# Kernel tuning notes

Hardware: AMD Instinct MI355X
Metric: run time of the kernel (lower is better)

Reference implementation:

```python
import jax, jax.numpy as jnp
import numpy as np

EPS = float(np.finfo(np.float32).eps)


def _m_step(padded, shifted, gp, B, K, C):
    # padded: [u, b=C+1, i, j]; shifted: [u, s, a=C, i, j]; gp: [u, k, i, j]
    ops_first = jnp.einsum('usaij,ukij,ubij->uskab', shifted, gp, padded)
    ops_second = jnp.einsum('uaij,ukij,ubij->ukab', padded, gp, padded)
    norm = 1.0 / jnp.einsum('ukaa->uk', ops_second)  # reciprocal of trace
    ops_first_n = ops_first * norm[:, None, :, None, None]
    eye_b = jnp.eye(C + 1, dtype=padded.dtype)
    ops_second_n = ops_second * norm[:, :, None, None] + EPS * eye_b
    ops = jnp.einsum('uskab,ukbc->uskac', ops_first_n, jnp.linalg.inv(ops_second_n))
    probs_norm = 1.0 / gp.sum(axis=(2, 3))
    pp = gp * probs_norm[:, :, None, None]
    # difference: [u, s, k, a, i, j]
    diff = shifted[:, :, None] - jnp.einsum('uskab,ubij->uskaij', ops, padded)
    eye_a = jnp.eye(C, dtype=padded.dtype)
    sigmas = jnp.einsum('uskaij,ukij,uskbij->uskab', diff, pp, diff) + EPS * eye_a
    return ops, sigmas


def _e_step(padded, shifted, ops, sigmas, B, K):
    diff = shifted[:, :, None] - jnp.einsum('uskab,ubij->uskaij', ops, padded)
    quad = jnp.einsum('uskaij,uskab,uskbij->ukij', diff, jnp.linalg.inv(sigmas), diff)
    _, logdet = jnp.linalg.slogdet(sigmas)  # sigmas is PD -> sign=+1
    return -0.5 * quad - 0.5 * logdet.sum(axis=1).reshape(B, K, 1, 1)


def em_forward(images, shifted_images, predicted_masks, em_steps):
    B, S, C, H, W = shifted_images.shape
    K = predicted_masks.shape[1]
    ones = jnp.ones((B, 1, H, W), dtype=images.dtype)
    padded = jnp.concatenate((images, ones), axis=1)  # [u, C+1, i, j]
    generated_masks = jnp.zeros_like(predicted_masks)
    for _ in range(em_steps):
        logits = jax.lax.stop_gradient(predicted_masks + generated_masks)
        gp = jax.nn.softmax(logits, axis=1) + EPS
        ops, sigmas = _m_step(jax.lax.stop_gradient(padded),
                              jax.lax.stop_gradient(shifted_images), gp, B, K, C)
        ops = jax.lax.stop_gradient(ops)
        sigmas = jax.lax.stop_gradient(sigmas)
        generated_masks = _e_step(padded, shifted_images, ops, sigmas, B, K)
    return generated_masks


def setup_inputs() -> dict:
    key = jax.random.key(0)
    k1, k2, k3 = jax.random.split(key, 3)
    B, S, C, H, W, K = 16, 8, 3, 128, 128, 6
    images = jax.random.uniform(k1, (B, C, H, W), dtype=jnp.float32)
    shifted_images = jax.random.uniform(k2, (B, S, C, H, W), dtype=jnp.float32)
    predicted_masks = jax.random.normal(k3, (B, K, H, W), dtype=jnp.float32)
    return {"images": images, "shifted_images": shifted_images,
            "predicted_masks": predicted_masks}


def reference(images, shifted_images, predicted_masks):
    return em_forward(images, shifted_images, predicted_masks, em_steps=3)
```

## Files before the change

kernel.cpp:

```cpp
#include <hip/hip_runtime.h>
#include <math.h>

#define EPSF 1.1920928955078125e-07f

constexpr int B_ = 16, S_ = 8, CH = 3, K_ = 6;
constexpr int P_ = 128 * 128;
constexpr int NCR = 4;
constexpr int NCE = 32;
constexpr int NF = 160;
constexpr int PW = 168;

__device__ __forceinline__ int swz8(int bid, int nwg) {
  return (bid & 7) * (nwg >> 3) + (bid >> 3);
}
__device__ __forceinline__ float4 ld4(const float* p) { return *(const float4*)p; }
__device__ __forceinline__ void st4(float* p, float4 v) { *(float4*)p = v; }
__device__ __forceinline__ float dot4(float4 a, float4 b) {
  return a.x * b.x + a.y * b.y + a.z * b.z + a.w * b.w;
}
__device__ __forceinline__ float sum4(float4 a) { return a.x + a.y + a.z + a.w; }
__device__ __forceinline__ float4 mul4(float4 a, float4 b) {
  return make_float4(a.x * b.x, a.y * b.y, a.z * b.z, a.w * b.w);
}
__device__ __forceinline__ float4 dcompv(float4 s, float4 i0, float4 i1, float4 i2,
                                         float4 o) {
  float4 r;
  r.x = s.x - (o.x * i0.x + o.y * i1.x + o.z * i2.x + o.w);
  r.y = s.y - (o.x * i0.y + o.y * i1.y + o.z * i2.y + o.w);
  r.z = s.z - (o.x * i0.z + o.y * i1.z + o.z * i2.z + o.w);
  r.w = s.w - (o.x * i0.w + o.y * i1.w + o.z * i2.w + o.w);
  return r;
}
__device__ __forceinline__ float quadv(float d0, float d1, float d2, float4 sA,
                                       float2 sB) {
  return sA.x * d0 * d0 + sA.y * d0 * d1 + sA.z * d0 * d2 + sA.w * d1 * d1 +
         sB.x * d1 * d2 + sB.y * d2 * d2;
}

__device__ __forceinline__ void inv4(const float* Ain, float* out) {
  float a[4][8];
#pragma unroll
  for (int i = 0; i < 4; i++) {
#pragma unroll
    for (int j = 0; j < 4; j++) { a[i][j] = Ain[i * 4 + j]; a[i][4 + j] = (i == j) ? 1.f : 0.f; }
  }
#pragma unroll
  for (int c = 0; c < 4; c++) {
    float piv = 1.f / a[c][c];
#pragma unroll
    for (int j = 0; j < 8; j++) a[c][j] *= piv;
#pragma unroll
    for (int r = 0; r < 4; r++) {
      if (r != c) {
        float f = a[r][c];
#pragma unroll
        for (int j = 0; j < 8; j++) a[r][j] -= f * a[c][j];
      }
    }
  }
#pragma unroll
  for (int i = 0; i < 4; i++)
#pragma unroll
    for (int j = 0; j < 4; j++) out[i * 4 + j] = a[i][4 + j];
}

__global__ __launch_bounds__(256) void k_softmax0(const float* __restrict__ pred,
                                                  float* __restrict__ gp) {
  int g = blockIdx.x * 256 + threadIdx.x;
  int u = g >> 14, p = g & (P_ - 1);
  const float* pr = pred + ((size_t)u * K_) * P_ + p;
  float l[K_];
  float mx = -1e30f;
#pragma unroll
  for (int k = 0; k < K_; k++) { l[k] = pr[(size_t)k * P_]; mx = fmaxf(mx, l[k]); }
  float s = 0.f;
#pragma unroll
  for (int k = 0; k < K_; k++) { l[k] = expf(l[k] - mx); s += l[k]; }
  float inv = 1.f / s;
  float* gw = gp + ((size_t)u * K_) * P_ + p;
#pragma unroll
  for (int k = 0; k < K_; k++) gw[(size_t)k * P_] = l[k] * inv + EPSF;
}

__global__ __launch_bounds__(256, 1) void k_moments(const float* __restrict__ img,
                                                    const float* __restrict__ shf,
                                                    const float* __restrict__ gp,
                                                    float* __restrict__ p1) {
  __shared__ float red[46][33];
  int wg = swz8(blockIdx.x, B_ * K_ * 4 * NCR);
  int u = wg / 96;
  int r = wg % 96;
  int k = r >> 4, sq = (r >> 2) & 3, ch = r & 3;
  int tid = threadIdx.x, lane = tid & 63, w = tid >> 6;

  const float* imgu = img + (size_t)u * CH * P_;
  const float* shfu = shf + ((size_t)u * S_ + sq * 2) * CH * P_;
  const float* gpu = gp + (size_t)(u * K_ + k) * P_;

  float acc[46];
#pragma unroll
  for (int i = 0; i < 46; i++) acc[i] = 0.f;

#pragma unroll
  for (int it = 0; it < 4; it++) {
    int p = ch * 4096 + it * 1024 + tid * 4;
    float4 i0 = ld4(imgu + p);
    float4 i1 = ld4(imgu + P_ + p);
    float4 i2 = ld4(imgu + 2 * P_ + p);
    float4 g = ld4(gpu + p);
    float4 t0 = mul4(g, i0), t1 = mul4(g, i1), t2 = mul4(g, i2);
#pragma unroll
    for (int ls = 0; ls < 2; ls++) {
      float4 s0 = ld4(shfu + (ls * 3 + 0) * P_ + p);
      float4 s1 = ld4(shfu + (ls * 3 + 1) * P_ + p);
      float4 s2 = ld4(shfu + (ls * 3 + 2) * P_ + p);
      int fb = ls * 12;
      acc[fb + 0] += dot4(s0, t0); acc[fb + 1] += dot4(s0, t1);
      acc[fb + 2] += dot4(s0, t2); acc[fb + 3] += dot4(s0, g);
      acc[fb + 4] += dot4(s1, t0); acc[fb + 5] += dot4(s1, t1);
      acc[fb + 6] += dot4(s1, t2); acc[fb + 7] += dot4(s1, g);
      acc[fb + 8] += dot4(s2, t0); acc[fb + 9] += dot4(s2, t1);
      acc[fb + 10] += dot4(s2, t2); acc[fb + 11] += dot4(s2, g);
      float4 gs0 = mul4(g, s0), gs1 = mul4(g, s1), gs2 = mul4(g, s2);
      int mb = 24 + ls * 6;
      acc[mb + 0] += dot4(gs0, s0); acc[mb + 1] += dot4(gs0, s1);
      acc[mb + 2] += dot4(gs0, s2); acc[mb + 3] += dot4(gs1, s1);
      acc[mb + 4] += dot4(gs1, s2); acc[mb + 5] += dot4(gs2, s2);
    }
    if (sq == 0) {
      acc[36] += dot4(i0, t0); acc[37] += dot4(i1, t0); acc[38] += dot4(i2, t0);
      acc[39] += sum4(t0);
      acc[40] += dot4(i1, t1); acc[41] += dot4(i2, t1); acc[42] += sum4(t1);
      acc[43] += dot4(i2, t2); acc[44] += sum4(t2);
      acc[45] += sum4(g);
    }
  }
#pragma unroll
  for (int j = 0; j < 46; j++) {
    float v = acc[j];
    v += __shfl_xor(v, 1, 64);
    v += __shfl_xor(v, 2, 64);
    v += __shfl_xor(v, 4, 64);
    acc[j] = v;
  }
  if ((lane & 7) == 0) {
    int col = w * 8 + (lane >> 3);
#pragma unroll
    for (int j = 0; j < 46; j++) red[j][col] = acc[j];
  }
  __syncthreads();
  if (tid < 46 && (tid < 36 || sq == 0)) {
    float s = 0.f;
#pragma unroll
    for (int c = 0; c < 32; c++) s += red[tid][c];
    int off = (tid < 24) ? (sq * 24 + tid)
                         : (tid < 36 ? (106 + sq * 12 + tid - 24) : (96 + tid - 36));
    p1[((size_t)(u * K_ + k) * NCR + ch) * NF + off] = s;
  }
}

__global__ __launch_bounds__(256) void k_solve(const float* __restrict__ p1,
                                               float* __restrict__ params) {
  __shared__ float sumL[K_][154];
  __shared__ float invAL[K_][16];
  __shared__ float OL[K_][96];
  __shared__ float normL[K_], pnL[K_];
  __shared__ float ldetL[K_ * S_];
  int u = blockIdx.x;
  int tid = threadIdx.x;

  for (int e = tid; e < K_ * 154; e += 256) {
    int k = e / 154, i = e % 154;
    const float* src = p1 + (size_t)(u * K_ + k) * NCR * NF + i;
    float s = 0.f;
#pragma unroll
    for (int c = 0; c < NCR; c++) s += src[c * NF];
    sumL[k][i] = s;
  }
  __syncthreads();
  if (tid < K_) {
    const float* m = &sumL[tid][96];
    float tr = m[0] + m[4] + m[7] + m[9];
    float nrm = 1.f / tr;
    normL[tid] = nrm;
    pnL[tid] = 1.f / m[9];
    const int sym[4][4] = {{0, 1, 2, 3}, {1, 4, 5, 6}, {2, 5, 7, 8}, {3, 6, 8, 9}};
    float A[16];
#pragma unroll
    for (int i = 0; i < 4; i++)
#pragma unroll
      for (int j = 0; j < 4; j++)
        A[i * 4 + j] = m[sym[i][j]] * nrm + ((i == j) ? EPSF : 0.f);
    inv4(A, invAL[tid]);
  }
  __syncthreads();
  for (int e = tid; e < K_ * 96; e += 256) {
    int k = e / 96, r = e % 96, sa = r >> 2, bc = r & 3;
    float v = 0.f;
#pragma unroll
    for (int c = 0; c < 4; c++) v += sumL[k][sa * 4 + c] * invAL[k][c * 4 + bc];
    v *= normL[k];
    OL[k][r] = v;
    params[(size_t)(u * K_ + k) * PW + r] = v;
  }
  __syncthreads();
  if (tid < K_ * S_) {
    int k = tid >> 3, s = tid & 7;
    const float* F = &sumL[k][s * 12];
    const float* O = &OL[k][s * 12];
    const float* M2 = &sumL[k][96];
    const float* Ms = &sumL[k][106 + s * 6];
    float pn = pnL[k];
    const int sym[4][4] = {{0, 1, 2, 3}, {1, 4, 5, 6}, {2, 5, 7, 8}, {3, 6, 8, 9}};
    float FO[9];
#pragma unroll
    for (int a = 0; a < 3; a++)
#pragma unroll
      for (int b = 0; b < 3; b++) {
        float v = 0.f;
#pragma unroll
        for (int c = 0; c < 4; c++) v += F[a * 4 + c] * O[b * 4 + c];
        FO[a * 3 + b] = v;
      }
    float W[12];
#pragma unroll
    for (int a = 0; a < 3; a++)
#pragma unroll
      for (int c = 0; c < 4; c++) {
        float v = 0.f;
#pragma unroll
        for (int d = 0; d < 4; d++) v += O[a * 4 + d] * M2[sym[d][c]];
        W[a * 4 + c] = v;
      }
    float OMO[6];
    {
      const int pa[6] = {0, 0, 0, 1, 1, 2}, pb[6] = {0, 1, 2, 1, 2, 2};
#pragma unroll
      for (int t = 0; t < 6; t++) {
        float v = 0.f;
#pragma unroll
        for (int c = 0; c < 4; c++) v += W[pa[t] * 4 + c] * O[pb[t] * 4 + c];
        OMO[t] = v;
      }
    }
    float a = pn * (Ms[0] - 2.f * FO[0] + OMO[0]) + EPSF;
    float b = pn * (Ms[1] - FO[1] - FO[3] + OMO[1]);
    float c = pn * (Ms[2] - FO[2] - FO[6] + OMO[2]);
    float d = pn * (Ms[3] - 2.f * FO[4] + OMO[3]) + EPSF;
    float e = pn * (Ms[4] - FO[5] - FO[7] + OMO[4]);
    float f = pn * (Ms[5] - 2.f * FO[8] + OMO[5]) + EPSF;
    float c00 = d * f - e * e, c01 = c * e - b * f, c02 = b * e - c * d;
    float det = a * c00 + b * c01 + c * c02;
    float id = 1.f / det;
    float* ps = params + (size_t)(u * K_ + k) * PW + 96 + s * 8;
    ps[0] = 0.5f * c00 * id;
    ps[1] = c01 * id;
    ps[2] = c02 * id;
    ps[3] = 0.5f * (a * f - c * c) * id;
    ps[4] = (c * b - a * e) * id;
    ps[5] = 0.5f * (a * d - b * b) * id;
    ldetL[tid] = logf(det);
  }
  __syncthreads();
  if (tid < K_) {
    float s = 0.f;
#pragma unroll
    for (int si = 0; si < S_; si++) s += ldetL[tid * S_ + si];
    params[(size_t)(u * K_ + tid) * PW + 160] = 0.5f * s;
  }
}

template <int LAST>
__global__ __launch_bounds__(768, 3) void k_estep(const float* __restrict__ img,
                                                  const float* __restrict__ shf,
                                                  const float* __restrict__ pred,
                                                  const float* __restrict__ params,
                                                  float* __restrict__ out,
                                                  float* __restrict__ gp) {
  __shared__ __align__(16) float pL[K_][PW];
  __shared__ __align__(16) float qL[K_][512];
  __shared__ __align__(16) float gmL[K_][512];

  int wg = swz8(blockIdx.x, B_ * NCE);
  int u = wg >> 5, ch = wg & 31;
  int tid = threadIdx.x, lane = tid & 63, w = tid >> 6;
  int k = w >> 1, shalf = w & 1;

  for (int e = tid; e < K_ * PW; e += 768)
    pL[e / PW][e % PW] = params[(size_t)u * K_ * PW + e];
  __syncthreads();

  const float* ob = &pL[k][shalf * 48];
  const float* sb = &pL[k][96 + shalf * 32];
  float ldh = pL[k][160];

  const float* imgu = img + (size_t)u * CH * P_;
  const float* shfu = shf + ((size_t)u * S_ + shalf * 4) * CH * P_;

  int p0 = ch * 512 + lane * 4;
  float4 i0a = ld4(imgu + p0),          i0b = ld4(imgu + p0 + 256);
  float4 i1a = ld4(imgu + P_ + p0),     i1b = ld4(imgu + P_ + p0 + 256);
  float4 i2a = ld4(imgu + 2 * P_ + p0), i2b = ld4(imgu + 2 * P_ + p0 + 256);
  float4 qa = make_float4(0.f, 0.f, 0.f, 0.f);
  float4 qb = make_float4(0.f, 0.f, 0.f, 0.f);
#pragma unroll
  for (int sl = 0; sl < 4; sl++) {
    float4 oA = ld4(ob + sl * 12 + 0);
    float4 oB = ld4(ob + sl * 12 + 4);
    float4 oC = ld4(ob + sl * 12 + 8);
    float4 sA = ld4(sb + sl * 8);
    float2 sB = *(const float2*)(sb + sl * 8 + 4);
    const float* s0 = shfu + (sl * 3 + 0) * P_;
    const float* s1 = shfu + (sl * 3 + 1) * P_;
    const float* s2 = shfu + (sl * 3 + 2) * P_;
    {
      float4 d0 = dcompv(ld4(s0 + p0), i0a, i1a, i2a, oA);
      float4 d1 = dcompv(ld4(s1 + p0), i0a, i1a, i2a, oB);
      float4 d2 = dcompv(ld4(s2 + p0), i0a, i1a, i2a, oC);
      qa.x += quadv(d0.x, d1.x, d2.x, sA, sB);
      qa.y += quadv(d0.y, d1.y, d2.y, sA, sB);
      qa.z += quadv(d0.z, d1.z, d2.z, sA, sB);
      qa.w += quadv(d0.w, d1.w, d2.w, sA, sB);
    }
    {
      float4 d0 = dcompv(ld4(s0 + p0 + 256), i0b, i1b, i2b, oA);
      float4 d1 = dcompv(ld4(s1 + p0 + 256), i0b, i1b, i2b, oB);
      float4 d2 = dcompv(ld4(s2 + p0 + 256), i0b, i1b, i2b, oC);
      qb.x += quadv(d0.x, d1.x, d2.x, sA, sB);
      qb.y += quadv(d0.y, d1.y, d2.y, sA, sB);
      qb.z += quadv(d0.z, d1.z, d2.z, sA, sB);
      qb.w += quadv(d0.w, d1.w, d2.w, sA, sB);
    }
  }
  int pxa = lane * 4, pxb = lane * 4 + 256;
  if (shalf == 1) {
    st4(&qL[k][pxa], qa);
    st4(&qL[k][pxb], qb);
  }
  __syncthreads();
  if (shalf == 0) {
    float* outu = out + (size_t)(u * K_ + k) * P_;
    float4 qha = ld4(&qL[k][pxa]);
    float4 qhb = ld4(&qL[k][pxb]);
    float4 g4a, g4b;
    g4a.x = -(qa.x + qha.x + ldh); g4a.y = -(qa.y + qha.y + ldh);
    g4a.z = -(qa.z + qha.z + ldh); g4a.w = -(qa.w + qha.w + ldh);
    g4b.x = -(qb.x + qhb.x + ldh); g4b.y = -(qb.y + qhb.y + ldh);
    g4b.z = -(qb.z + qhb.z + ldh); g4b.w = -(qb.w + qhb.w + ldh);
    st4(outu + ch * 512 + pxa, g4a);
    st4(outu + ch * 512 + pxb, g4b);
    if constexpr (!LAST) {
      st4(&gmL[k][pxa], g4a);
      st4(&gmL[k][pxb], g4b);
    }
  }
  if constexpr (!LAST) {
    __syncthreads();
    if (tid < 512) {
      int p = ch * 512 + tid;
      const float* predu = pred + (size_t)u * K_ * P_;
      float* gpu = gp + (size_t)u * K_ * P_;
      float l[K_];
      float mx = -1e30f;
#pragma unroll
      for (int k2 = 0; k2 < K_; k2++) {
        l[k2] = predu[(size_t)k2 * P_ + p] + gmL[k2][tid];
        mx = fmaxf(mx, l[k2]);
      }
      float ss = 0.f;
#pragma unroll
      for (int k2 = 0; k2 < K_; k2++) { l[k2] = expf(l[k2] - mx); ss += l[k2]; }
      float inv = 1.f / ss;
#pragma unroll
      for (int k2 = 0; k2 < K_; k2++) gpu[(size_t)k2 * P_ + p] = l[k2] * inv + EPSF;
    }
  }
}

extern "C" void kernel_launch(void* const* d_in, const int* in_sizes, int n_in,
                              void* d_out, int out_size, void* d_ws, size_t ws_size,
                              hipStream_t stream) {
  const float* img = (const float*)d_in[0];
  const float* shf = (const float*)d_in[1];
  const float* pred = (const float*)d_in[2];
  float* out = (float*)d_out;
  float* wsf = (float*)d_ws;
  float* gp = wsf;
  float* p1 = gp + (size_t)B_ * K_ * P_;
  float* params = p1 + (size_t)B_ * K_ * NCR * NF;

  k_softmax0<<<(B_ * P_) / 256, 256, 0, stream>>>(pred, gp);
  for (int step = 0; step < 3; step++) {
    k_moments<<<B_ * K_ * 4 * NCR, 256, 0, stream>>>(img, shf, gp, p1);
    k_solve<<<B_, 256, 0, stream>>>(p1, params);
    if (step < 2)
      k_estep<0><<<B_ * NCE, 768, 0, stream>>>(img, shf, pred, params, out, gp);
    else
      k_estep<1><<<B_ * NCE, 768, 0, stream>>>(img, shf, pred, params, out, gp);
  }
}
```

Before: 144.2 us.

## Fuse E-step, softmax and moment accumulation into one kernel per EM step

Merges the E-step, the softmax that builds gp, and the M-step moment reductions into a single templated kernel. gp now stays in shared memory instead of going through a global workspace, and the separate softmax0 and moments launches are dropped. Each block now accumulates 82 partial sums over its 512-pixel chunk, so there are 32 partial slices per (u,k) for k_solve to reduce instead of 4. The cost is higher register pressure (launch bounds 768,1), which lowers occupancy, plus more partial sums to reduce in k_solve.

```diff
diff --git a/kernel.cpp b/kernel.cpp
--- a/kernel.cpp
+++ b/kernel.cpp
@@ -5,10 +5,10 @@
 
 constexpr int B_ = 16, S_ = 8, CH = 3, K_ = 6;
 constexpr int P_ = 128 * 128;
-constexpr int NCR = 4;
 constexpr int NCE = 32;
 constexpr int NF = 160;
 constexpr int PW = 168;
+constexpr int NACC = 82;
 
 __device__ __forceinline__ int swz8(int bid, int nwg) {
   return (bid & 7) * (nwg >> 3) + (bid >> 3);
@@ -64,98 +64,191 @@
     for (int j = 0; j < 4; j++) out[i * 4 + j] = a[i][4 + j];
 }
 
-__global__ __launch_bounds__(256) void k_softmax0(const float* __restrict__ pred,
-                                                  float* __restrict__ gp) {
-  int g = blockIdx.x * 256 + threadIdx.x;
-  int u = g >> 14, p = g & (P_ - 1);
-  const float* pr = pred + ((size_t)u * K_) * P_ + p;
-  float l[K_];
-  float mx = -1e30f;
-#pragma unroll
-  for (int k = 0; k < K_; k++) { l[k] = pr[(size_t)k * P_]; mx = fmaxf(mx, l[k]); }
-  float s = 0.f;
-#pragma unroll
-  for (int k = 0; k < K_; k++) { l[k] = expf(l[k] - mx); s += l[k]; }
-  float inv = 1.f / s;
-  float* gw = gp + ((size_t)u * K_) * P_ + p;
-#pragma unroll
-  for (int k = 0; k < K_; k++) gw[(size_t)k * P_] = l[k] * inv + EPSF;
-}
-
-__global__ __launch_bounds__(256, 1) void k_moments(const float* __restrict__ img,
-                                                    const float* __restrict__ shf,
-                                                    const float* __restrict__ gp,
-                                                    float* __restrict__ p1) {
-  __shared__ float red[46][33];
-  int wg = swz8(blockIdx.x, B_ * K_ * 4 * NCR);
-  int u = wg / 96;
-  int r = wg % 96;
-  int k = r >> 4, sq = (r >> 2) & 3, ch = r & 3;
+template <int MODE>
+__global__ __launch_bounds__(768, 1) void k_fused(const float* __restrict__ img,
+                                                  const float* __restrict__ shf,
+                                                  const float* __restrict__ pred,
+                                                  const float* __restrict__ params,
+                                                  float* __restrict__ out,
+                                                  float* __restrict__ p1) {
+  __shared__ __align__(16) float pL[K_][PW];
+  __shared__ __align__(16) float qL[(MODE >= 1) ? K_ * 512 : 1];
+  __shared__ __align__(16) float gmL[K_][512];
+  __shared__ float redM[(MODE <= 1) ? 12 * NACC * 5 : 1];
+
+  int wg = swz8(blockIdx.x, B_ * NCE);
+  int u = wg >> 5, ch = wg & 31;
   int tid = threadIdx.x, lane = tid & 63, w = tid >> 6;
+  int k = w >> 1, shalf = w & 1;
 
   const float* imgu = img + (size_t)u * CH * P_;
-  const float* shfu = shf + ((size_t)u * S_ + sq * 2) * CH * P_;
-  const float* gpu = gp + (size_t)(u * K_ + k) * P_;
-
-  float acc[46];
-#pragma unroll
-  for (int i = 0; i < 46; i++) acc[i] = 0.f;
-
-#pragma unroll
-  for (int it = 0; it < 4; it++) {
-    int p = ch * 4096 + it * 1024 + tid * 4;
-    float4 i0 = ld4(imgu + p);
-    float4 i1 = ld4(imgu + P_ + p);
-    float4 i2 = ld4(imgu + 2 * P_ + p);
-    float4 g = ld4(gpu + p);
-    float4 t0 = mul4(g, i0), t1 = mul4(g, i1), t2 = mul4(g, i2);
-#pragma unroll
-    for (int ls = 0; ls < 2; ls++) {
-      float4 s0 = ld4(shfu + (ls * 3 + 0) * P_ + p);
-      float4 s1 = ld4(shfu + (ls * 3 + 1) * P_ + p);
-      float4 s2 = ld4(shfu + (ls * 3 + 2) * P_ + p);
-      int fb = ls * 12;
-      acc[fb + 0] += dot4(s0, t0); acc[fb + 1] += dot4(s0, t1);
-      acc[fb + 2] += dot4(s0, t2); acc[fb + 3] += dot4(s0, g);
-      acc[fb + 4] += dot4(s1, t0); acc[fb + 5] += dot4(s1, t1);
-      acc[fb + 6] += dot4(s1, t2); acc[fb + 7] += dot4(s1, g);
-      acc[fb + 8] += dot4(s2, t0); acc[fb + 9] += dot4(s2, t1);
-      acc[fb + 10] += dot4(s2, t2); acc[fb + 11] += dot4(s2, g);
-      float4 gs0 = mul4(g, s0), gs1 = mul4(g, s1), gs2 = mul4(g, s2);
-      int mb = 24 + ls * 6;
-      acc[mb + 0] += dot4(gs0, s0); acc[mb + 1] += dot4(gs0, s1);
-      acc[mb + 2] += dot4(gs0, s2); acc[mb + 3] += dot4(gs1, s1);
-      acc[mb + 4] += dot4(gs1, s2); acc[mb + 5] += dot4(gs2, s2);
-    }
-    if (sq == 0) {
-      acc[36] += dot4(i0, t0); acc[37] += dot4(i1, t0); acc[38] += dot4(i2, t0);
-      acc[39] += sum4(t0);
-      acc[40] += dot4(i1, t1); acc[41] += dot4(i2, t1); acc[42] += sum4(t1);
-      acc[43] += dot4(i2, t2); acc[44] += sum4(t2);
-      acc[45] += sum4(g);
-    }
-  }
-#pragma unroll
-  for (int j = 0; j < 46; j++) {
-    float v = acc[j];
-    v += __shfl_xor(v, 1, 64);
-    v += __shfl_xor(v, 2, 64);
-    v += __shfl_xor(v, 4, 64);
-    acc[j] = v;
-  }
-  if ((lane & 7) == 0) {
-    int col = w * 8 + (lane >> 3);
-#pragma unroll
-    for (int j = 0; j < 46; j++) red[j][col] = acc[j];
-  }
-  __syncthreads();
-  if (tid < 46 && (tid < 36 || sq == 0)) {
-    float s = 0.f;
-#pragma unroll
-    for (int c = 0; c < 32; c++) s += red[tid][c];
-    int off = (tid < 24) ? (sq * 24 + tid)
-                         : (tid < 36 ? (106 + sq * 12 + tid - 24) : (96 + tid - 36));
-    p1[((size_t)(u * K_ + k) * NCR + ch) * NF + off] = s;
+  const float* shfu = shf + ((size_t)u * S_ + shalf * 4) * CH * P_;
+  const float* predu = pred + (size_t)u * K_ * P_;
+  int p0 = ch * 512 + lane * 4;
+  int pxa = lane * 4, pxb = lane * 4 + 256;
+
+  if constexpr (MODE >= 1) {
+    for (int e = tid; e < K_ * PW; e += 768)
+      pL[e / PW][e % PW] = params[(size_t)u * K_ * PW + e];
+    __syncthreads();
+
+    const float* ob = &pL[k][shalf * 48];
+    const float* sb = &pL[k][96 + shalf * 32];
+    float ldh = pL[k][160];
+
+    float4 i0a = ld4(imgu + p0),          i0b = ld4(imgu + p0 + 256);
+    float4 i1a = ld4(imgu + P_ + p0),     i1b = ld4(imgu + P_ + p0 + 256);
+    float4 i2a = ld4(imgu + 2 * P_ + p0), i2b = ld4(imgu + 2 * P_ + p0 + 256);
+    float4 qa = make_float4(0.f, 0.f, 0.f, 0.f);
+    float4 qb = make_float4(0.f, 0.f, 0.f, 0.f);
+#pragma unroll
+    for (int sl = 0; sl < 4; sl++) {
+      float4 oA = ld4(ob + sl * 12 + 0);
+      float4 oB = ld4(ob + sl * 12 + 4);
+      float4 oC = ld4(ob + sl * 12 + 8);
+      float4 sA = ld4(sb + sl * 8);
+      float2 sB = *(const float2*)(sb + sl * 8 + 4);
+      const float* s0 = shfu + (sl * 3 + 0) * P_;
+      const float* s1 = shfu + (sl * 3 + 1) * P_;
+      const float* s2 = shfu + (sl * 3 + 2) * P_;
+      {
+        float4 d0 = dcompv(ld4(s0 + p0), i0a, i1a, i2a, oA);
+        float4 d1 = dcompv(ld4(s1 + p0), i0a, i1a, i2a, oB);
+        float4 d2 = dcompv(ld4(s2 + p0), i0a, i1a, i2a, oC);
+        qa.x += quadv(d0.x, d1.x, d2.x, sA, sB);
+        qa.y += quadv(d0.y, d1.y, d2.y, sA, sB);
+        qa.z += quadv(d0.z, d1.z, d2.z, sA, sB);
+        qa.w += quadv(d0.w, d1.w, d2.w, sA, sB);
+      }
+      {
+        float4 d0 = dcompv(ld4(s0 + p0 + 256), i0b, i1b, i2b, oA);
+        float4 d1 = dcompv(ld4(s1 + p0 + 256), i0b, i1b, i2b, oB);
+        float4 d2 = dcompv(ld4(s2 + p0 + 256), i0b, i1b, i2b, oC);
+        qb.x += quadv(d0.x, d1.x, d2.x, sA, sB);
+        qb.y += quadv(d0.y, d1.y, d2.y, sA, sB);
+        qb.z += quadv(d0.z, d1.z, d2.z, sA, sB);
+        qb.w += quadv(d0.w, d1.w, d2.w, sA, sB);
+      }
+    }
+    if (shalf == 1) {
+      st4(&qL[k * 512 + pxa], qa);
+      st4(&qL[k * 512 + pxb], qb);
+    }
+    __syncthreads();
+    if (shalf == 0) {
+      float4 qha = ld4(&qL[k * 512 + pxa]);
+      float4 qhb = ld4(&qL[k * 512 + pxb]);
+      float4 g4a, g4b;
+      g4a.x = -(qa.x + qha.x + ldh); g4a.y = -(qa.y + qha.y + ldh);
+      g4a.z = -(qa.z + qha.z + ldh); g4a.w = -(qa.w + qha.w + ldh);
+      g4b.x = -(qb.x + qhb.x + ldh); g4b.y = -(qb.y + qhb.y + ldh);
+      g4b.z = -(qb.z + qhb.z + ldh); g4b.w = -(qb.w + qhb.w + ldh);
+      if constexpr (MODE == 2) {
+        float* outu = out + (size_t)(u * K_ + k) * P_;
+        st4(outu + ch * 512 + pxa, g4a);
+        st4(outu + ch * 512 + pxb, g4b);
+      } else {
+        st4(&gmL[k][pxa], g4a);
+        st4(&gmL[k][pxb], g4b);
+      }
+    }
+    if constexpr (MODE == 2) return;
+    __syncthreads();
+  }
+
+  if constexpr (MODE <= 1) {
+    if (tid < 512) {
+      int p = ch * 512 + tid;
+      float l[K_];
+      float mx = -1e30f;
+#pragma unroll
+      for (int k2 = 0; k2 < K_; k2++) {
+        l[k2] = predu[(size_t)k2 * P_ + p];
+        if constexpr (MODE == 1) l[k2] += gmL[k2][tid];
+        mx = fmaxf(mx, l[k2]);
+      }
+      float ss = 0.f;
+#pragma unroll
+      for (int k2 = 0; k2 < K_; k2++) { l[k2] = expf(l[k2] - mx); ss += l[k2]; }
+      float inv = 1.f / ss;
+#pragma unroll
+      for (int k2 = 0; k2 < K_; k2++) gmL[k2][tid] = l[k2] * inv + EPSF;
+    }
+    __syncthreads();
+    asm volatile("" ::: "memory");
+
+    float acc[NACC];
+#pragma unroll
+    for (int i = 0; i < NACC; i++) acc[i] = 0.f;
+#pragma unroll
+    for (int it = 0; it < 2; it++) {
+      int p = p0 + it * 256;
+      int px = lane * 4 + it * 256;
+      float4 i0 = ld4(imgu + p);
+      float4 i1 = ld4(imgu + P_ + p);
+      float4 i2 = ld4(imgu + 2 * P_ + p);
+      float4 g = ld4(&gmL[k][px]);
+      float4 t0 = mul4(g, i0), t1 = mul4(g, i1), t2 = mul4(g, i2);
+#pragma unroll
+      for (int ls = 0; ls < 4; ls++) {
+        float4 s0 = ld4(shfu + (ls * 3 + 0) * P_ + p);
+        float4 s1 = ld4(shfu + (ls * 3 + 1) * P_ + p);
+        float4 s2 = ld4(shfu + (ls * 3 + 2) * P_ + p);
+        int fb = ls * 12;
+        acc[fb + 0] += dot4(s0, t0); acc[fb + 1] += dot4(s0, t1);
+        acc[fb + 2] += dot4(s0, t2); acc[fb + 3] += dot4(s0, g);
+        acc[fb + 4] += dot4(s1, t0); acc[fb + 5] += dot4(s1, t1);
+        acc[fb + 6] += dot4(s1, t2); acc[fb + 7] += dot4(s1, g);
+        acc[fb + 8] += dot4(s2, t0); acc[fb + 9] += dot4(s2, t1);
+        acc[fb + 10] += dot4(s2, t2); acc[fb + 11] += dot4(s2, g);
+        float4 gs0 = mul4(g, s0), gs1 = mul4(g, s1), gs2 = mul4(g, s2);
+        int mb = 48 + ls * 6;
+        acc[mb + 0] += dot4(gs0, s0); acc[mb + 1] += dot4(gs0, s1);
+        acc[mb + 2] += dot4(gs0, s2); acc[mb + 3] += dot4(gs1, s1);
+        acc[mb + 4] += dot4(gs1, s2); acc[mb + 5] += dot4(gs2, s2);
+      }
+      if (shalf == 0) {
+        acc[72] += dot4(i0, t0); acc[73] += dot4(i1, t0); acc[74] += dot4(i2, t0);
+        acc[75] += sum4(t0);
+        acc[76] += dot4(i1, t1); acc[77] += dot4(i2, t1); acc[78] += sum4(t1);
+        acc[79] += dot4(i2, t2); acc[80] += sum4(t2);
+        acc[81] += sum4(g);
+      }
+    }
+#pragma unroll
+    for (int j = 0; j < NACC; j++) {
+      float v = acc[j];
+      v += __shfl_xor(v, 1, 64);
+      v += __shfl_xor(v, 2, 64);
+      v += __shfl_xor(v, 4, 64);
+      v += __shfl_xor(v, 8, 64);
+      acc[j] = v;
+    }
+    __syncthreads();
+    if ((lane & 15) == 0) {
+      int col = lane >> 4;
+#pragma unroll
+      for (int j = 0; j < NACC; j++) redM[(w * NACC + j) * 5 + col] = acc[j];
+    }
+    __syncthreads();
+    for (int e = tid; e < 12 * NACC; e += 768) {
+      int ww = e / NACC, j = e % NACC;
+      int kk = ww >> 1, sh = ww & 1;
+      if (sh && j >= 72) continue;
+      float s = redM[e * 5 + 0] + redM[e * 5 + 1] + redM[e * 5 + 2] + redM[e * 5 + 3];
+      int off;
+      if (j < 48) {
+        int ss2 = sh * 4 + j / 12;
+        off = ss2 * 12 + (j % 12);
+      } else if (j < 72) {
+        int t = j - 48;
+        int ss2 = sh * 4 + t / 6;
+        off = 106 + ss2 * 6 + (t % 6);
+      } else {
+        off = 96 + (j - 72);
+      }
+      p1[((size_t)(u * K_ + kk) * NCE + ch) * NF + off] = s;
+    }
   }
 }
 
@@ -171,10 +264,10 @@
 
   for (int e = tid; e < K_ * 154; e += 256) {
     int k = e / 154, i = e % 154;
-    const float* src = p1 + (size_t)(u * K_ + k) * NCR * NF + i;
+    const float* src = p1 + (size_t)(u * K_ + k) * NCE * NF + i;
     float s = 0.f;
 #pragma unroll
-    for (int c = 0; c < NCR; c++) s += src[c * NF];
+    for (int c = 0; c < NCE; c++) s += src[c * NF];
     sumL[k][i] = s;
   }
   __syncthreads();
@@ -270,113 +363,6 @@
   }
 }
 
-template <int LAST>
-__global__ __launch_bounds__(768, 3) void k_estep(const float* __restrict__ img,
-                                                  const float* __restrict__ shf,
-                                                  const float* __restrict__ pred,
-                                                  const float* __restrict__ params,
-                                                  float* __restrict__ out,
-                                                  float* __restrict__ gp) {
-  __shared__ __align__(16) float pL[K_][PW];
-  __shared__ __align__(16) float qL[K_][512];
-  __shared__ __align__(16) float gmL[K_][512];
-
-  int wg = swz8(blockIdx.x, B_ * NCE);
-  int u = wg >> 5, ch = wg & 31;
-  int tid = threadIdx.x, lane = tid & 63, w = tid >> 6;
-  int k = w >> 1, shalf = w & 1;
-
-  for (int e = tid; e < K_ * PW; e += 768)
-    pL[e / PW][e % PW] = params[(size_t)u * K_ * PW + e];
-  __syncthreads();
-
-  const float* ob = &pL[k][shalf * 48];
-  const float* sb = &pL[k][96 + shalf * 32];
-  float ldh = pL[k][160];
-
-  const float* imgu = img + (size_t)u * CH * P_;
-  const float* shfu = shf + ((size_t)u * S_ + shalf * 4) * CH * P_;
-
-  int p0 = ch * 512 + lane * 4;
-  float4 i0a = ld4(imgu + p0),          i0b = ld4(imgu + p0 + 256);
-  float4 i1a = ld4(imgu + P_ + p0),     i1b = ld4(imgu + P_ + p0 + 256);
-  float4 i2a = ld4(imgu + 2 * P_ + p0), i2b = ld4(imgu + 2 * P_ + p0 + 256);
-  float4 qa = make_float4(0.f, 0.f, 0.f, 0.f);
-  float4 qb = make_float4(0.f, 0.f, 0.f, 0.f);
-#pragma unroll
-  for (int sl = 0; sl < 4; sl++) {
-    float4 oA = ld4(ob + sl * 12 + 0);
-    float4 oB = ld4(ob + sl * 12 + 4);
-    float4 oC = ld4(ob + sl * 12 + 8);
-    float4 sA = ld4(sb + sl * 8);
-    float2 sB = *(const float2*)(sb + sl * 8 + 4);
-    const float* s0 = shfu + (sl * 3 + 0) * P_;
-    const float* s1 = shfu + (sl * 3 + 1) * P_;
-    const float* s2 = shfu + (sl * 3 + 2) * P_;
-    {
-      float4 d0 = dcompv(ld4(s0 + p0), i0a, i1a, i2a, oA);
-      float4 d1 = dcompv(ld4(s1 + p0), i0a, i1a, i2a, oB);
-      float4 d2 = dcompv(ld4(s2 + p0), i0a, i1a, i2a, oC);
-      qa.x += quadv(d0.x, d1.x, d2.x, sA, sB);
-      qa.y += quadv(d0.y, d1.y, d2.y, sA, sB);
-      qa.z += quadv(d0.z, d1.z, d2.z, sA, sB);
-      qa.w += quadv(d0.w, d1.w, d2.w, sA, sB);
-    }
-    {
-      float4 d0 = dcompv(ld4(s0 + p0 + 256), i0b, i1b, i2b, oA);
-      float4 d1 = dcompv(ld4(s1 + p0 + 256), i0b, i1b, i2b, oB);
-      float4 d2 = dcompv(ld4(s2 + p0 + 256), i0b, i1b, i2b, oC);
-      qb.x += quadv(d0.x, d1.x, d2.x, sA, sB);
-      qb.y += quadv(d0.y, d1.y, d2.y, sA, sB);
-      qb.z += quadv(d0.z, d1.z, d2.z, sA, sB);
-      qb.w += quadv(d0.w, d1.w, d2.w, sA, sB);
-    }
-  }
-  int pxa = lane * 4, pxb = lane * 4 + 256;
-  if (shalf == 1) {
-    st4(&qL[k][pxa], qa);
-    st4(&qL[k][pxb], qb);
-  }
-  __syncthreads();
-  if (shalf == 0) {
-    float* outu = out + (size_t)(u * K_ + k) * P_;
-    float4 qha = ld4(&qL[k][pxa]);
-    float4 qhb = ld4(&qL[k][pxb]);
-    float4 g4a, g4b;
-    g4a.x = -(qa.x + qha.x + ldh); g4a.y = -(qa.y + qha.y + ldh);
-    g4a.z = -(qa.z + qha.z + ldh); g4a.w = -(qa.w + qha.w + ldh);
-    g4b.x = -(qb.x + qhb.x + ldh); g4b.y = -(qb.y + qhb.y + ldh);
-    g4b.z = -(qb.z + qhb.z + ldh); g4b.w = -(qb.w + qhb.w + ldh);
-    st4(outu + ch * 512 + pxa, g4a);
-    st4(outu + ch * 512 + pxb, g4b);
-    if constexpr (!LAST) {
-      st4(&gmL[k][pxa], g4a);
-      st4(&gmL[k][pxb], g4b);
-    }
-  }
-  if constexpr (!LAST) {
-    __syncthreads();
-    if (tid < 512) {
-      int p = ch * 512 + tid;
-      const float* predu = pred + (size_t)u * K_ * P_;
-      float* gpu = gp + (size_t)u * K_ * P_;
-      float l[K_];
-      float mx = -1e30f;
-#pragma unroll
-      for (int k2 = 0; k2 < K_; k2++) {
-        l[k2] = predu[(size_t)k2 * P_ + p] + gmL[k2][tid];
-        mx = fmaxf(mx, l[k2]);
-      }
-      float ss = 0.f;
-#pragma unroll
-      for (int k2 = 0; k2 < K_; k2++) { l[k2] = expf(l[k2] - mx); ss += l[k2]; }
-      float inv = 1.f / ss;
-#pragma unroll
-      for (int k2 = 0; k2 < K_; k2++) gpu[(size_t)k2 * P_ + p] = l[k2] * inv + EPSF;
-    }
-  }
-}
-
 extern "C" void kernel_launch(void* const* d_in, const int* in_sizes, int n_in,
                               void* d_out, int out_size, void* d_ws, size_t ws_size,
                               hipStream_t stream) {
@@ -385,17 +371,14 @@
   const float* pred = (const float*)d_in[2];
   float* out = (float*)d_out;
   float* wsf = (float*)d_ws;
-  float* gp = wsf;
-  float* p1 = gp + (size_t)B_ * K_ * P_;
-  float* params = p1 + (size_t)B_ * K_ * NCR * NF;
-
-  k_softmax0<<<(B_ * P_) / 256, 256, 0, stream>>>(pred, gp);
-  for (int step = 0; step < 3; step++) {
-    k_moments<<<B_ * K_ * 4 * NCR, 256, 0, stream>>>(img, shf, gp, p1);
-    k_solve<<<B_, 256, 0, stream>>>(p1, params);
-    if (step < 2)
-      k_estep<0><<<B_ * NCE, 768, 0, stream>>>(img, shf, pred, params, out, gp);
-    else
-      k_estep<1><<<B_ * NCE, 768, 0, stream>>>(img, shf, pred, params, out, gp);
-  }
-}
+  float* p1 = wsf;
+  float* params = p1 + (size_t)B_ * K_ * NCE * NF;
+
+  k_fused<0><<<B_ * NCE, 768, 0, stream>>>(img, shf, pred, nullptr, nullptr, p1);
+  k_solve<<<B_, 256, 0, stream>>>(p1, params);
+  k_fused<1><<<B_ * NCE, 768, 0, stream>>>(img, shf, pred, params, nullptr, p1);
+  k_solve<<<B_, 256, 0, stream>>>(p1, params);
+  k_fused<1><<<B_ * NCE, 768, 0, stream>>>(img, shf, pred, params, nullptr, p1);
+  k_solve<<<B_, 256, 0, stream>>>(p1, params);
+  k_fused<2><<<B_ * NCE, 768, 0, stream>>>(img, shf, pred, params, out, p1);
+}
```

New measurement: 228.3 us. 58.3% more time.

## Restructure moments kernel to one workgroup per pixel chunk covering all K

Applied to the files above, without the earlier changes.

Replaces the moments kernel that launched one workgroup per (batch, k, shift-quad, chunk) with one 384-thread workgroup per (batch, 512-pixel chunk). Each wave handles one mixture component and loops over the four shift groups. This cuts repeated image loads across k and matches the e-step's chunking, but it produces 32 partial rows per component, so the solve kernel has to sum more partials. It also stops writing the output tensor in the non-final e-steps, since only the last step's values are kept.

```diff
diff --git a/kernel.cpp b/kernel.cpp
--- a/kernel.cpp
+++ b/kernel.cpp
@@ -5,10 +5,10 @@
 
 constexpr int B_ = 16, S_ = 8, CH = 3, K_ = 6;
 constexpr int P_ = 128 * 128;
-constexpr int NCR = 4;
-constexpr int NCE = 32;
+constexpr int NCH = 32;
 constexpr int NF = 160;
 constexpr int PW = 168;
+
 
 __device__ __forceinline__ int swz8(int bid, int nwg) {
   return (bid & 7) * (nwg >> 3) + (bid >> 3);
@@ -68,94 +68,100 @@
                                                   float* __restrict__ gp) {
   int g = blockIdx.x * 256 + threadIdx.x;
   int u = g >> 14, p = g & (P_ - 1);
-  const float* pr = pred + ((size_t)u * K_) * P_ + p;
+  size_t base = ((size_t)u * K_) * P_ + p;
   float l[K_];
   float mx = -1e30f;
 #pragma unroll
-  for (int k = 0; k < K_; k++) { l[k] = pr[(size_t)k * P_]; mx = fmaxf(mx, l[k]); }
+  for (int k = 0; k < K_; k++) { l[k] = pred[base + (size_t)k * P_]; mx = fmaxf(mx, l[k]); }
   float s = 0.f;
 #pragma unroll
   for (int k = 0; k < K_; k++) { l[k] = expf(l[k] - mx); s += l[k]; }
   float inv = 1.f / s;
-  float* gw = gp + ((size_t)u * K_) * P_ + p;
-#pragma unroll
-  for (int k = 0; k < K_; k++) gw[(size_t)k * P_] = l[k] * inv + EPSF;
-}
-
-__global__ __launch_bounds__(256, 1) void k_moments(const float* __restrict__ img,
-                                                    const float* __restrict__ shf,
-                                                    const float* __restrict__ gp,
-                                                    float* __restrict__ p1) {
-  __shared__ float red[46][33];
-  int wg = swz8(blockIdx.x, B_ * K_ * 4 * NCR);
-  int u = wg / 96;
-  int r = wg % 96;
-  int k = r >> 4, sq = (r >> 2) & 3, ch = r & 3;
-  int tid = threadIdx.x, lane = tid & 63, w = tid >> 6;
+#pragma unroll
+  for (int k = 0; k < K_; k++) gp[base + (size_t)k * P_] = l[k] * inv + EPSF;
+}
+
+__global__ __launch_bounds__(384, 1) void k_mom(const float* __restrict__ img,
+                                                const float* __restrict__ shf,
+                                                const float* __restrict__ gp,
+                                                float* __restrict__ p1) {
+  __shared__ float red[K_][46][5];
+  int wg = swz8(blockIdx.x, B_ * NCH);
+  int u = wg >> 5, ch = wg & 31;
+  int tid = threadIdx.x, lane = tid & 63, k = tid >> 6;
 
   const float* imgu = img + (size_t)u * CH * P_;
-  const float* shfu = shf + ((size_t)u * S_ + sq * 2) * CH * P_;
+  const float* shfu = shf + (size_t)u * S_ * CH * P_;
   const float* gpu = gp + (size_t)(u * K_ + k) * P_;
-
-  float acc[46];
-#pragma unroll
-  for (int i = 0; i < 46; i++) acc[i] = 0.f;
-
-#pragma unroll
-  for (int it = 0; it < 4; it++) {
-    int p = ch * 4096 + it * 1024 + tid * 4;
-    float4 i0 = ld4(imgu + p);
-    float4 i1 = ld4(imgu + P_ + p);
-    float4 i2 = ld4(imgu + 2 * P_ + p);
-    float4 g = ld4(gpu + p);
-    float4 t0 = mul4(g, i0), t1 = mul4(g, i1), t2 = mul4(g, i2);
-#pragma unroll
-    for (int ls = 0; ls < 2; ls++) {
-      float4 s0 = ld4(shfu + (ls * 3 + 0) * P_ + p);
-      float4 s1 = ld4(shfu + (ls * 3 + 1) * P_ + p);
-      float4 s2 = ld4(shfu + (ls * 3 + 2) * P_ + p);
-      int fb = ls * 12;
-      acc[fb + 0] += dot4(s0, t0); acc[fb + 1] += dot4(s0, t1);
-      acc[fb + 2] += dot4(s0, t2); acc[fb + 3] += dot4(s0, g);
-      acc[fb + 4] += dot4(s1, t0); acc[fb + 5] += dot4(s1, t1);
-      acc[fb + 6] += dot4(s1, t2); acc[fb + 7] += dot4(s1, g);
-      acc[fb + 8] += dot4(s2, t0); acc[fb + 9] += dot4(s2, t1);
-      acc[fb + 10] += dot4(s2, t2); acc[fb + 11] += dot4(s2, g);
-      float4 gs0 = mul4(g, s0), gs1 = mul4(g, s1), gs2 = mul4(g, s2);
-      int mb = 24 + ls * 6;
-      acc[mb + 0] += dot4(gs0, s0); acc[mb + 1] += dot4(gs0, s1);
-      acc[mb + 2] += dot4(gs0, s2); acc[mb + 3] += dot4(gs1, s1);
-      acc[mb + 4] += dot4(gs1, s2); acc[mb + 5] += dot4(gs2, s2);
-    }
-    if (sq == 0) {
-      acc[36] += dot4(i0, t0); acc[37] += dot4(i1, t0); acc[38] += dot4(i2, t0);
-      acc[39] += sum4(t0);
-      acc[40] += dot4(i1, t1); acc[41] += dot4(i2, t1); acc[42] += sum4(t1);
-      acc[43] += dot4(i2, t2); acc[44] += sum4(t2);
-      acc[45] += sum4(g);
-    }
-  }
-#pragma unroll
-  for (int j = 0; j < 46; j++) {
-    float v = acc[j];
-    v += __shfl_xor(v, 1, 64);
-    v += __shfl_xor(v, 2, 64);
-    v += __shfl_xor(v, 4, 64);
-    acc[j] = v;
-  }
-  if ((lane & 7) == 0) {
-    int col = w * 8 + (lane >> 3);
-#pragma unroll
-    for (int j = 0; j < 46; j++) red[j][col] = acc[j];
-  }
-  __syncthreads();
-  if (tid < 46 && (tid < 36 || sq == 0)) {
-    float s = 0.f;
-#pragma unroll
-    for (int c = 0; c < 32; c++) s += red[tid][c];
-    int off = (tid < 24) ? (sq * 24 + tid)
-                         : (tid < 36 ? (106 + sq * 12 + tid - 24) : (96 + tid - 36));
-    p1[((size_t)(u * K_ + k) * NCR + ch) * NF + off] = s;
+  int p0 = ch * 512 + lane * 4;
+
+#pragma unroll 1
+  for (int sq = 0; sq < 4; sq++) {
+    const float* shq = shfu + sq * 2 * CH * P_;
+    float acc[46];
+#pragma unroll
+    for (int i = 0; i < 46; i++) acc[i] = 0.f;
+#pragma unroll
+    for (int it = 0; it < 2; it++) {
+      int p = p0 + it * 256;
+      float4 i0 = ld4(imgu + p);
+      float4 i1 = ld4(imgu + P_ + p);
+      float4 i2 = ld4(imgu + 2 * P_ + p);
+      float4 g = ld4(gpu + p);
+      float4 t0 = mul4(g, i0), t1 = mul4(g, i1), t2 = mul4(g, i2);
+#pragma unroll
+      for (int ls = 0; ls < 2; ls++) {
+        float4 s0 = ld4(shq + (ls * 3 + 0) * P_ + p);
+        float4 s1 = ld4(shq + (ls * 3 + 1) * P_ + p);
+        float4 s2 = ld4(shq + (ls * 3 + 2) * P_ + p);
+        int fb = ls * 12;
+        acc[fb + 0] += dot4(s0, t0); acc[fb + 1] += dot4(s0, t1);
+        acc[fb + 2] += dot4(s0, t2); acc[fb + 3] += dot4(s0, g);
+        acc[fb + 4] += dot4(s1, t0); acc[fb + 5] += dot4(s1, t1);
+        acc[fb + 6] += dot4(s1, t2); acc[fb + 7] += dot4(s1, g);
+        acc[fb + 8] += dot4(s2, t0); acc[fb + 9] += dot4(s2, t1);
+        acc[fb + 10] += dot4(s2, t2); acc[fb + 11] += dot4(s2, g);
+        float4 gs0 = mul4(g, s0), gs1 = mul4(g, s1), gs2 = mul4(g, s2);
+        int mb = 24 + ls * 6;
+        acc[mb + 0] += dot4(gs0, s0); acc[mb + 1] += dot4(gs0, s1);
+        acc[mb + 2] += dot4(gs0, s2); acc[mb + 3] += dot4(gs1, s1);
+        acc[mb + 4] += dot4(gs1, s2); acc[mb + 5] += dot4(gs2, s2);
+      }
+      if (sq == 0) {
+        acc[36] += dot4(i0, t0); acc[37] += dot4(i1, t0); acc[38] += dot4(i2, t0);
+        acc[39] += sum4(t0);
+        acc[40] += dot4(i1, t1); acc[41] += dot4(i2, t1); acc[42] += sum4(t1);
+        acc[43] += dot4(i2, t2); acc[44] += sum4(t2);
+        acc[45] += sum4(g);
+      }
+    }
+    int n = (sq == 0) ? 46 : 36;
+#pragma unroll
+    for (int j = 0; j < 46; j++) {
+      if (j >= n) break;
+      float v = acc[j];
+      v += __shfl_xor(v, 1, 64);
+      v += __shfl_xor(v, 2, 64);
+      v += __shfl_xor(v, 4, 64);
+      v += __shfl_xor(v, 8, 64);
+      acc[j] = v;
+    }
+    if ((lane & 15) == 0) {
+      int col = lane >> 4;
+#pragma unroll
+      for (int j = 0; j < 46; j++) {
+        if (j >= n) break;
+        red[k][j][col] = acc[j];
+      }
+    }
+    if (lane < n) {
+      float s = red[k][lane][0] + red[k][lane][1] + red[k][lane][2] + red[k][lane][3];
+      int off;
+      if (lane < 24) off = (sq * 2 + lane / 12) * 12 + (lane % 12);
+      else if (lane < 36) off = 106 + (sq * 2 + (lane - 24) / 6) * 6 + ((lane - 24) % 6);
+      else off = 96 + (lane - 36);
+      p1[((size_t)(u * K_ + k) * NCH + ch) * NF + off] = s;
+    }
   }
 }
 
@@ -171,10 +177,10 @@
 
   for (int e = tid; e < K_ * 154; e += 256) {
     int k = e / 154, i = e % 154;
-    const float* src = p1 + (size_t)(u * K_ + k) * NCR * NF + i;
+    const float* src = p1 + (size_t)(u * K_ + k) * NCH * NF + i;
     float s = 0.f;
 #pragma unroll
-    for (int c = 0; c < NCR; c++) s += src[c * NF];
+    for (int c = 0; c < NCH; c++) s += src[c * NF];
     sumL[k][i] = s;
   }
   __syncthreads();
@@ -277,27 +283,29 @@
                                                   const float* __restrict__ params,
                                                   float* __restrict__ out,
                                                   float* __restrict__ gp) {
-  __shared__ __align__(16) float pL[K_][PW];
-  __shared__ __align__(16) float qL[K_][512];
+  __shared__ __align__(16) float pL[K_ * PW];
+  __shared__ __align__(16) float qL[K_ * 512];
   __shared__ __align__(16) float gmL[K_][512];
 
-  int wg = swz8(blockIdx.x, B_ * NCE);
+  int wg = swz8(blockIdx.x, B_ * NCH);
   int u = wg >> 5, ch = wg & 31;
   int tid = threadIdx.x, lane = tid & 63, w = tid >> 6;
   int k = w >> 1, shalf = w & 1;
 
   for (int e = tid; e < K_ * PW; e += 768)
-    pL[e / PW][e % PW] = params[(size_t)u * K_ * PW + e];
-  __syncthreads();
-
-  const float* ob = &pL[k][shalf * 48];
-  const float* sb = &pL[k][96 + shalf * 32];
-  float ldh = pL[k][160];
+    pL[e] = params[(size_t)u * K_ * PW + e];
+  __syncthreads();
+
+  const float* ob = &pL[k * PW + shalf * 48];
+  const float* sb = &pL[k * PW + 96 + shalf * 32];
+  float ldh = pL[k * PW + 160];
 
   const float* imgu = img + (size_t)u * CH * P_;
   const float* shfu = shf + ((size_t)u * S_ + shalf * 4) * CH * P_;
-
+  const float* predu = pred + (size_t)u * K_ * P_;
   int p0 = ch * 512 + lane * 4;
+  int pxa = lane * 4, pxb = lane * 4 + 256;
+
   float4 i0a = ld4(imgu + p0),          i0b = ld4(imgu + p0 + 256);
   float4 i1a = ld4(imgu + P_ + p0),     i1b = ld4(imgu + P_ + p0 + 256);
   float4 i2a = ld4(imgu + 2 * P_ + p0), i2b = ld4(imgu + 2 * P_ + p0 + 256);
@@ -332,24 +340,24 @@
       qb.w += quadv(d0.w, d1.w, d2.w, sA, sB);
     }
   }
-  int pxa = lane * 4, pxb = lane * 4 + 256;
   if (shalf == 1) {
-    st4(&qL[k][pxa], qa);
-    st4(&qL[k][pxb], qb);
+    st4(&qL[k * 512 + pxa], qa);
+    st4(&qL[k * 512 + pxb], qb);
   }
   __syncthreads();
   if (shalf == 0) {
-    float* outu = out + (size_t)(u * K_ + k) * P_;
-    float4 qha = ld4(&qL[k][pxa]);
-    float4 qhb = ld4(&qL[k][pxb]);
+    float4 qha = ld4(&qL[k * 512 + pxa]);
+    float4 qhb = ld4(&qL[k * 512 + pxb]);
     float4 g4a, g4b;
     g4a.x = -(qa.x + qha.x + ldh); g4a.y = -(qa.y + qha.y + ldh);
     g4a.z = -(qa.z + qha.z + ldh); g4a.w = -(qa.w + qha.w + ldh);
     g4b.x = -(qb.x + qhb.x + ldh); g4b.y = -(qb.y + qhb.y + ldh);
     g4b.z = -(qb.z + qhb.z + ldh); g4b.w = -(qb.w + qhb.w + ldh);
-    st4(outu + ch * 512 + pxa, g4a);
-    st4(outu + ch * 512 + pxb, g4b);
-    if constexpr (!LAST) {
+    if constexpr (LAST) {
+      float* outu = out + (size_t)(u * K_ + k) * P_;
+      st4(outu + ch * 512 + pxa, g4a);
+      st4(outu + ch * 512 + pxb, g4b);
+    } else {
       st4(&gmL[k][pxa], g4a);
       st4(&gmL[k][pxb], g4b);
     }
@@ -358,7 +366,6 @@
     __syncthreads();
     if (tid < 512) {
       int p = ch * 512 + tid;
-      const float* predu = pred + (size_t)u * K_ * P_;
       float* gpu = gp + (size_t)u * K_ * P_;
       float l[K_];
       float mx = -1e30f;
@@ -387,15 +394,15 @@
   float* wsf = (float*)d_ws;
   float* gp = wsf;
   float* p1 = gp + (size_t)B_ * K_ * P_;
-  float* params = p1 + (size_t)B_ * K_ * NCR * NF;
+  float* params = p1 + (size_t)B_ * K_ * NCH * NF;
 
   k_softmax0<<<(B_ * P_) / 256, 256, 0, stream>>>(pred, gp);
   for (int step = 0; step < 3; step++) {
-    k_moments<<<B_ * K_ * 4 * NCR, 256, 0, stream>>>(img, shf, gp, p1);
+    k_mom<<<B_ * NCH, 384, 0, stream>>>(img, shf, gp, p1);
     k_solve<<<B_, 256, 0, stream>>>(p1, params);
     if (step < 2)
-      k_estep<0><<<B_ * NCE, 768, 0, stream>>>(img, shf, pred, params, out, gp);
+      k_estep<0><<<B_ * NCH, 768, 0, stream>>>(img, shf, pred, params, nullptr, gp);
     else
-      k_estep<1><<<B_ * NCE, 768, 0, stream>>>(img, shf, pred, params, out, gp);
-  }
-}
+      k_estep<1><<<B_ * NCH, 768, 0, stream>>>(img, shf, pred, params, out, nullptr);
+  }
+}
```

Measured after the change: 420.8 us. 2.92x slower.
